# Performance work log

Hardware: AMD Instinct MI355X
Metric: run time of the kernel (lower is better)

The kernel has to match this reference:

```python
import jax, jax.numpy as jnp
import numpy as np

DIM = 1024
HEADS = 16
SCALE = DIM ** -0.5  # note: source scales by full dim, not head dim


def setup_inputs() -> dict:
    key = jax.random.key(0)
    k1, k2, k3 = jax.random.split(key, 3)
    b, n = 2, 2048
    x = jax.random.normal(k1, (b, n, DIM), dtype=jnp.float32)
    w_qkv = jax.random.normal(k2, (3 * DIM, DIM), dtype=jnp.float32) * (DIM ** -0.5)
    w_out = jax.random.normal(k3, (DIM, DIM), dtype=jnp.float32) * (DIM ** -0.5)
    b_out = jnp.zeros((DIM,), dtype=jnp.float32)
    return {"x": x, "w_qkv": w_qkv, "w_out": w_out, "b_out": b_out}


def reference(x, w_qkv, w_out, b_out):
    b, n, d = x.shape
    h = HEADS
    hd = d // h
    # torch Linear: y = x @ W.T
    qkv = x @ w_qkv.T  # [b, n, 3d]
    q, k, v = jnp.split(qkv, 3, axis=-1)
    # reshape to [b, h, n, hd]
    def to_heads(t):
        return t.reshape(b, n, h, hd).transpose(0, 2, 1, 3)
    q, k, v = to_heads(q), to_heads(k), to_heads(v)
    dots = jnp.einsum('bhqd,bhkd->bhqk', q, k) * SCALE
    attn = jax.nn.softmax(dots, axis=-1)
    out = jnp.einsum('bhqk,bhkd->bhqd', attn, v)
    out = out.transpose(0, 2, 1, 3).reshape(b, n, d)
    return out @ w_out.T + b_out
```

## Files before the change

kernel.cpp:

```cpp
#include <hip/hip_runtime.h>

typedef __attribute__((ext_vector_type(8))) _Float16 half8;
typedef __attribute__((ext_vector_type(4))) _Float16 half4;
typedef __attribute__((ext_vector_type(2))) __fp16 fp16x2;
typedef __attribute__((ext_vector_type(4))) float f32x4;
typedef __attribute__((ext_vector_type(4))) unsigned int u32x4;
typedef __attribute__((ext_vector_type(2))) unsigned int u32x2;

#define NSEQ 2048
#define DIMM 1024
#define NH   16
#define HD   64

typedef const void __attribute__((address_space(1))) gvoid_t;
typedef void __attribute__((address_space(3))) svoid_t;

__device__ __forceinline__ void gload_lds16(const void* g, void* l) {
  __builtin_amdgcn_global_load_lds((gvoid_t*)g, (svoid_t*)l, 16, 0, 0);
}

union H2U { fp16x2 h; unsigned int u; };

__global__ __launch_bounds__(256) void cvt_all(const float* __restrict__ x,
                                               const float* __restrict__ wqkv,
                                               const float* __restrict__ wout,
                                               _Float16* __restrict__ xh,
                                               _Float16* __restrict__ wqkvh,
                                               _Float16* __restrict__ wouth) {
  int i = blockIdx.x * 256 + threadIdx.x;
  const float* src;
  _Float16* dst;
  int off;
  if (i < 524288) { src = x; dst = xh; off = i; }
  else if (i < 917504) { src = wqkv; dst = wqkvh; off = i - 524288; }
  else { src = wout; dst = wouth; off = i - 917504; }
  const float4* p = (const float4*)src + (size_t)off * 2;
  float4 v0 = p[0], v1 = p[1];
  half8 h;
  h[0] = (_Float16)v0.x; h[1] = (_Float16)v0.y; h[2] = (_Float16)v0.z; h[3] = (_Float16)v0.w;
  h[4] = (_Float16)v1.x; h[5] = (_Float16)v1.y; h[6] = (_Float16)v1.z; h[7] = (_Float16)v1.w;
  *((half8*)dst + off) = h;
}

__device__ __forceinline__ void gemm_mainloop(const _Float16* __restrict__ A,
                                              const _Float16* __restrict__ B,
                                              int am0, int bn0,
                                              _Float16* As, _Float16* Bs,
                                              f32x4 acc[4][4]) {
  const int tid = threadIdx.x;
  const int w = tid >> 6, lane = tid & 63;
  const int lr = lane >> 2;
  const int lc = (lane & 3) * 8;
  const int wm = (w >> 1) * 64, wn = (w & 1) * 64;
  const int g = lane >> 4, ln = lane & 15;

  for (int k0 = 0; k0 < 1024; k0 += 32) {
#pragma unroll
    for (int rr = 0; rr < 4; ++rr) {
      int c = rr * 4 + w;
      if (c < 8) {
        gload_lds16(A + (size_t)(am0 + c * 16 + lr) * 1024 + k0 + lc, As + c * 512);
      } else {
        int cb = c - 8;
        gload_lds16(B + (size_t)(bn0 + cb * 16 + lr) * 1024 + k0 + lc, Bs + cb * 512);
      }
    }
    __syncthreads();
    half8 af[4], bf[4];
#pragma unroll
    for (int mi = 0; mi < 4; ++mi)
      af[mi] = *(const half8*)(As + (wm + mi * 16 + ln) * 32 + g * 8);
#pragma unroll
    for (int ni = 0; ni < 4; ++ni)
      bf[ni] = *(const half8*)(Bs + (wn + ni * 16 + ln) * 32 + g * 8);
#pragma unroll
    for (int mi = 0; mi < 4; ++mi)
#pragma unroll
      for (int ni = 0; ni < 4; ++ni)
        acc[mi][ni] = __builtin_amdgcn_mfma_f32_16x16x32_f16(af[mi], bf[ni], acc[mi][ni], 0, 0, 0);
    __syncthreads();
  }
}

union SmemQKV {
  struct { _Float16 a[128 * 32]; _Float16 b[128 * 32]; } ab;
  _Float16 t[128 * 136];
};

#define QSCALE 0.0450843450f

__global__ __launch_bounds__(256) void gemm_qkv(const _Float16* __restrict__ x,
                                                const _Float16* __restrict__ wqkv,
                                                _Float16* __restrict__ qh,
                                                _Float16* __restrict__ kh,
                                                _Float16* __restrict__ vt) {
  __shared__ SmemQKV sh;
  f32x4 acc[4][4];
#pragma unroll
  for (int i = 0; i < 4; ++i)
#pragma unroll
    for (int j = 0; j < 4; ++j) acc[i][j] = (f32x4){0.f, 0.f, 0.f, 0.f};
  const int bm = blockIdx.x, bn = blockIdx.y;
  gemm_mainloop(x, wqkv, bm * 128, bn * 128, sh.ab.a, sh.ab.b, acc);

  const int tid = threadIdx.x;
  const int w = tid >> 6, lane = tid & 63;
  const int g = lane >> 4, ln = lane & 15;
  const int wm = (w >> 1) * 64, wn = (w & 1) * 64;
  const int sec = bn >> 3;
  const int cbase = (bn & 7) * 128;

  if (sec < 2) {
    _Float16* dst = (sec == 0) ? qh : kh;
    const float scale = (sec == 0) ? QSCALE : 1.0f;
#pragma unroll
    for (int mi = 0; mi < 4; ++mi) {
      int row = bm * 128 + wm + mi * 16 + g * 4;
      int bidx = row >> 11, nidx = row & 2047;
#pragma unroll
      for (int ni = 0; ni < 4; ++ni) {
        int col = cbase + wn + ni * 16 + ln;
        int h = col >> 6, d = col & 63;
        _Float16* p = dst + ((size_t)(bidx * NH + h) * NSEQ + nidx) * HD + d;
#pragma unroll
        for (int r = 0; r < 4; ++r) p[r * HD] = (_Float16)(acc[mi][ni][r] * scale);
      }
    }
  } else {
    __syncthreads();
#pragma unroll
    for (int mi = 0; mi < 4; ++mi)
#pragma unroll
      for (int ni = 0; ni < 4; ++ni)
#pragma unroll
        for (int r = 0; r < 4; ++r)
          sh.t[(wn + ni * 16 + ln) * 136 + wm + mi * 16 + g * 4 + r] = (_Float16)acc[mi][ni][r];
    __syncthreads();
    const int row0 = bm * 128;
    const int bidx = row0 >> 11, n0 = row0 & 2047;
#pragma unroll
    for (int i = 0; i < 8; ++i) {
      int ci = i * 256 + tid;
      int drow = ci >> 4, nofs = (ci & 15) * 8;
      int col = cbase + drow;
      int h = col >> 6, d = col & 63;
      u32x4 val = *(const u32x4*)(sh.t + drow * 136 + nofs);
      *(u32x4*)(vt + ((size_t)(bidx * NH + h) * HD + d) * NSEQ + n0 + nofs) = val;
    }
  }
}

__global__ __launch_bounds__(256, 2) void attn_fwd(const _Float16* __restrict__ qh,
                                                   const _Float16* __restrict__ kh,
                                                   const _Float16* __restrict__ vt,
                                                   _Float16* __restrict__ ao) {
  __shared__ _Float16 Ks[2][64 * 64];
  __shared__ _Float16 Vs[2][64 * 64];
  __shared__ _Float16 Ps[4][32 * 64];

  const int bid = blockIdx.x;
  const int swz = (bid & 7) * 64 + (bid >> 3);
  const int bh = swz >> 4, qt = swz & 15;
  const int tid = threadIdx.x, w = tid >> 6, lane = tid & 63;
  const int g = lane >> 4, ln = lane & 15;
  const int sw8 = ln & 7;

  const _Float16* qp = qh + (size_t)bh * NSEQ * HD;
  const _Float16* kp = kh + (size_t)bh * NSEQ * HD;
  const _Float16* vp = vt + (size_t)bh * HD * NSEQ;
  char* psw = (char*)&Ps[w][0];

  const int qr = qt * 128 + w * 32;

  half8 qf[2][2];
#pragma unroll
  for (int qb = 0; qb < 2; ++qb)
#pragma unroll
    for (int dk = 0; dk < 2; ++dk)
      qf[qb][dk] = *(const half8*)(qp + (size_t)(qr + qb * 16 + ln) * HD + dk * 32 + g * 8);
  asm volatile("" ::: "memory");

  const int rsub = lane >> 3;
  const int csw = ((lane & 7) ^ rsub) << 3;
  const int c0 = 2 * w;

#define STAGE(buf, tt)                                                              \
  {                                                                                 \
    const _Float16* kt_ = kp + (size_t)(tt) * 64 * HD;                              \
    _Pragma("unroll")                                                               \
    for (int i = 0; i < 2; ++i) {                                                   \
      int c = c0 + i;                                                               \
      gload_lds16(kt_ + (size_t)(c * 8 + rsub) * HD + csw, &Ks[buf][c * 512]);      \
    }                                                                               \
    _Pragma("unroll")                                                               \
    for (int i = 0; i < 2; ++i) {                                                   \
      int c = c0 + i;                                                               \
      gload_lds16(vp + (size_t)(c * 8 + rsub) * NSEQ + (tt) * 64 + csw,             \
                  &Vs[buf][c * 512]);                                               \
    }                                                                               \
  }

  STAGE(0, 0);

  float lsum[2] = {0.f, 0.f};
  f32x4 oacc[4][2];
#pragma unroll
  for (int sd = 0; sd < 4; ++sd)
#pragma unroll
    for (int qb = 0; qb < 2; ++qb) oacc[sd][qb] = (f32x4){0.f, 0.f, 0.f, 0.f};
  const f32x4 fz = (f32x4){0.f, 0.f, 0.f, 0.f};

  for (int t = 0; t < 32; ++t) {
    const int cur = t & 1;
    STAGE(cur ^ 1, (t + 1) & 31);
    asm volatile("s_waitcnt vmcnt(4)" ::: "memory");
    __builtin_amdgcn_s_barrier();

    f32x4 sacc[4][2];
    __builtin_amdgcn_s_setprio(1);
#pragma unroll
    for (int s = 0; s < 4; ++s) {
      const _Float16* kb = &Ks[cur][(s * 16 + ln) * 64];
      half8 kf0 = *(const half8*)(kb + ((g ^ sw8) << 3));
      half8 kf1 = *(const half8*)(kb + (((4 + g) ^ sw8) << 3));
      sacc[s][0] = __builtin_amdgcn_mfma_f32_16x16x32_f16(kf0, qf[0][0], fz, 0, 0, 0);
      sacc[s][0] = __builtin_amdgcn_mfma_f32_16x16x32_f16(kf1, qf[0][1], sacc[s][0], 0, 0, 0);
      sacc[s][1] = __builtin_amdgcn_mfma_f32_16x16x32_f16(kf0, qf[1][0], fz, 0, 0, 0);
      sacc[s][1] = __builtin_amdgcn_mfma_f32_16x16x32_f16(kf1, qf[1][1], sacc[s][1], 0, 0, 0);
    }
    __builtin_amdgcn_s_setprio(0);

#pragma unroll
    for (int qb = 0; qb < 2; ++qb) {
      const int q = qb * 16 + ln;
      float rs = 0.f;
#pragma unroll
      for (int s = 0; s < 4; ++s) {
        float e0 = __builtin_amdgcn_exp2f(sacc[s][qb][0]);
        float e1 = __builtin_amdgcn_exp2f(sacc[s][qb][1]);
        float e2 = __builtin_amdgcn_exp2f(sacc[s][qb][2]);
        float e3 = __builtin_amdgcn_exp2f(sacc[s][qb][3]);
        rs += (e0 + e1) + (e2 + e3);
        H2U a, b2;
        a.h = __builtin_amdgcn_cvt_pkrtz(e0, e1);
        b2.h = __builtin_amdgcn_cvt_pkrtz(e2, e3);
        u32x2 quad; quad[0] = a.u; quad[1] = b2.u;
        const int kq = s * 4 + g;
        *(u32x2*)(psw + q * 128 + ((kq ^ ln) << 3)) = quad;
      }
      lsum[qb] += rs;
    }
    asm volatile("s_waitcnt lgkmcnt(0)" ::: "memory");

    half8 pb[2][2];
#pragma unroll
    for (int qb = 0; qb < 2; ++qb) {
      const int q = qb * 16 + ln;
#pragma unroll
      for (int f = 0; f < 2; ++f) {
        const int qd = (f * 4 + g) * 2;
        u32x2 lo = *(const u32x2*)(psw + q * 128 + ((qd ^ ln) << 3));
        u32x2 hi = *(const u32x2*)(psw + q * 128 + (((qd + 1) ^ ln) << 3));
        union { u32x4 u; half8 h; } pk;
        pk.u[0] = lo[0]; pk.u[1] = lo[1]; pk.u[2] = hi[0]; pk.u[3] = hi[1];
        pb[qb][f] = pk.h;
      }
    }

    __builtin_amdgcn_s_setprio(1);
#pragma unroll
    for (int sd = 0; sd < 4; ++sd) {
      const _Float16* vb = &Vs[cur][(sd * 16 + ln) * 64];
      half8 vf0 = *(const half8*)(vb + ((g ^ sw8) << 3));
      half8 vf1 = *(const half8*)(vb + (((4 + g) ^ sw8) << 3));
#pragma unroll
      for (int qb = 0; qb < 2; ++qb) {
        oacc[sd][qb] = __builtin_amdgcn_mfma_f32_16x16x32_f16(vf0, pb[qb][0], oacc[sd][qb], 0, 0, 0);
        oacc[sd][qb] = __builtin_amdgcn_mfma_f32_16x16x32_f16(vf1, pb[qb][1], oacc[sd][qb], 0, 0, 0);
      }
    }
    __builtin_amdgcn_s_setprio(0);

    asm volatile("s_waitcnt lgkmcnt(0)" ::: "memory");
    __builtin_amdgcn_s_barrier();
  }

  const int bidx = bh >> 4, h = bh & 15;
#pragma unroll
  for (int qb = 0; qb < 2; ++qb) {
    lsum[qb] += __shfl_xor(lsum[qb], 16, 64);
    lsum[qb] += __shfl_xor(lsum[qb], 32, 64);
    const float inv = 1.f / lsum[qb];
    const int n = qr + qb * 16 + ln;
#pragma unroll
    for (int sd = 0; sd < 4; ++sd) {
      half4 o4;
#pragma unroll
      for (int r = 0; r < 4; ++r) o4[r] = (_Float16)(oacc[sd][qb][r] * inv);
      *(half4*)(ao + (size_t)(bidx * NSEQ + n) * DIMM + h * HD + sd * 16 + g * 4) = o4;
    }
  }
}

__global__ __launch_bounds__(256) void gemm_out(const _Float16* __restrict__ ao,
                                                const _Float16* __restrict__ wout,
                                                const float* __restrict__ bias,
                                                float* __restrict__ out) {
  __shared__ _Float16 As[128 * 32];
  __shared__ _Float16 Bs[128 * 32];
  f32x4 acc[4][4];
#pragma unroll
  for (int i = 0; i < 4; ++i)
#pragma unroll
    for (int j = 0; j < 4; ++j) acc[i][j] = (f32x4){0.f, 0.f, 0.f, 0.f};
  const int bm = blockIdx.x, bn = blockIdx.y;
  gemm_mainloop(ao, wout, bm * 128, bn * 128, As, Bs, acc);
  const int tid = threadIdx.x;
  const int w = tid >> 6, lane = tid & 63;
  const int g = lane >> 4, ln = lane & 15;
  const int wm = (w >> 1) * 64, wn = (w & 1) * 64;
#pragma unroll
  for (int mi = 0; mi < 4; ++mi) {
    const int row = bm * 128 + wm + mi * 16 + g * 4;
#pragma unroll
    for (int ni = 0; ni < 4; ++ni) {
      const int col = bn * 128 + wn + ni * 16 + ln;
      const float b = bias[col];
#pragma unroll
      for (int r = 0; r < 4; ++r) out[(size_t)(row + r) * DIMM + col] = acc[mi][ni][r] + b;
    }
  }
}

extern "C" void kernel_launch(void* const* d_in, const int* in_sizes, int n_in,
                              void* d_out, int out_size, void* d_ws, size_t ws_size,
                              hipStream_t stream) {
  const float* x    = (const float*)d_in[0];
  const float* wqkv = (const float*)d_in[1];
  const float* wout = (const float*)d_in[2];
  const float* bout = (const float*)d_in[3];
  float* out = (float*)d_out;

  _Float16* ws = (_Float16*)d_ws;
  _Float16* x_h    = ws;
  _Float16* wqkv_h = ws + (4u << 20);
  _Float16* wout_h = ws + (7u << 20);
  _Float16* q_h    = ws + (8u << 20);
  _Float16* k_h    = ws + (12u << 20);
  _Float16* vt_h   = ws + (16u << 20);
  _Float16* ao_h   = ws + (20u << 20);

  cvt_all<<<dim3(4096), 256, 0, stream>>>(x, wqkv, wout, x_h, wqkv_h, wout_h);
  gemm_qkv<<<dim3(32, 24), 256, 0, stream>>>(x_h, wqkv_h, q_h, k_h, vt_h);
  attn_fwd<<<dim3(512), 256, 0, stream>>>(q_h, k_h, vt_h, ao_h);
  gemm_out<<<dim3(32, 8), 256, 0, stream>>>(ao_h, wout_h, bout, out);
}
```

Baseline: 115.9 us.

## Split attention waves across key halves with 64-row query blocks and LDS reduction

Restructures the attention work split so each wave handles 64 query rows against one 32-key half of each K/V tile, instead of 32 query rows against the full tile. Each wave now loads fewer K/V fragments from LDS per MFMA and reads its P fragment as a single 16-byte load, which cuts LDS traffic and removes the packing shuffles. At the end, the two key-half partial outputs and row sums are combined through a shared-memory union buffer. The cost is more accumulator registers per wave (16 f32x4 output tiles), an extra end-of-kernel LDS reduction with a sync, and a risk of lower occupancy under launch_bounds(256,2).

```diff
diff --git a/kernel.cpp b/kernel.cpp
--- a/kernel.cpp
+++ b/kernel.cpp
@@ -150,13 +150,19 @@
   }
 }
 
-__global__ __launch_bounds__(256, 2) void attn_fwd(const _Float16* __restrict__ qh,
-                                                   const _Float16* __restrict__ kh,
-                                                   const _Float16* __restrict__ vt,
+union SmemPO {
+  _Float16 P[4][64 * 40];
+  float O[2][64][64];
+};
+
+__global__ __launch_bounds__(256, 2) void attn_fwd(const _Float16* __restrict__ qg,
+                                                   const _Float16* __restrict__ kg,
+                                                   const _Float16* __restrict__ vg,
                                                    _Float16* __restrict__ ao) {
   __shared__ _Float16 Ks[2][64 * 64];
   __shared__ _Float16 Vs[2][64 * 64];
-  __shared__ _Float16 Ps[4][32 * 64];
+  __shared__ SmemPO PO;
+  __shared__ float Lred[2][128];
 
   const int bid = blockIdx.x;
   const int swz = (bid & 7) * 64 + (bid >> 3);
@@ -164,20 +170,23 @@
   const int tid = threadIdx.x, w = tid >> 6, lane = tid & 63;
   const int g = lane >> 4, ln = lane & 15;
   const int sw8 = ln & 7;
-
-  const _Float16* qp = qh + (size_t)bh * NSEQ * HD;
-  const _Float16* kp = kh + (size_t)bh * NSEQ * HD;
-  const _Float16* vp = vt + (size_t)bh * HD * NSEQ;
-  char* psw = (char*)&Ps[w][0];
-
-  const int qr = qt * 128 + w * 32;
-
-  half8 qf[2][2];
-#pragma unroll
-  for (int qb = 0; qb < 2; ++qb)
+  const int kh2 = w & 1;
+  const int qh2 = w >> 1;
+  const int koff = kh2 * 32;
+
+  const _Float16* qp = qg + (size_t)bh * NSEQ * HD;
+  const _Float16* kp = kg + (size_t)bh * NSEQ * HD;
+  const _Float16* vp = vg + (size_t)bh * HD * NSEQ;
+  char* psw = (char*)&PO.P[w][0];
+
+  const int qr0 = qt * 128;
+
+  half8 qf[4][2];
+#pragma unroll
+  for (int qb = 0; qb < 4; ++qb)
 #pragma unroll
     for (int dk = 0; dk < 2; ++dk)
-      qf[qb][dk] = *(const half8*)(qp + (size_t)(qr + qb * 16 + ln) * HD + dk * 32 + g * 8);
+      qf[qb][dk] = *(const half8*)(qp + (size_t)(qr0 + qh2 * 64 + qb * 16 + ln) * HD + dk * 32 + g * 8);
   asm volatile("" ::: "memory");
 
   const int rsub = lane >> 3;
@@ -202,12 +211,12 @@
 
   STAGE(0, 0);
 
-  float lsum[2] = {0.f, 0.f};
-  f32x4 oacc[4][2];
-#pragma unroll
-  for (int sd = 0; sd < 4; ++sd)
-#pragma unroll
-    for (int qb = 0; qb < 2; ++qb) oacc[sd][qb] = (f32x4){0.f, 0.f, 0.f, 0.f};
+  float lsum[4] = {0.f, 0.f, 0.f, 0.f};
+  f32x4 oacc[4][4];
+#pragma unroll
+  for (int db = 0; db < 4; ++db)
+#pragma unroll
+    for (int qb = 0; qb < 4; ++qb) oacc[db][qb] = (f32x4){0.f, 0.f, 0.f, 0.f};
   const f32x4 fz = (f32x4){0.f, 0.f, 0.f, 0.f};
 
   for (int t = 0; t < 32; ++t) {
@@ -216,68 +225,58 @@
     asm volatile("s_waitcnt vmcnt(4)" ::: "memory");
     __builtin_amdgcn_s_barrier();
 
-    f32x4 sacc[4][2];
+    half8 kf[2][2];
+#pragma unroll
+    for (int kb = 0; kb < 2; ++kb)
+#pragma unroll
+      for (int dk = 0; dk < 2; ++dk)
+        kf[kb][dk] = *(const half8*)(&Ks[cur][0] + (koff + kb * 16 + ln) * 64 +
+                                     (((dk * 4 + g) ^ sw8) << 3));
+    f32x4 sacc[2][4];
     __builtin_amdgcn_s_setprio(1);
 #pragma unroll
-    for (int s = 0; s < 4; ++s) {
-      const _Float16* kb = &Ks[cur][(s * 16 + ln) * 64];
-      half8 kf0 = *(const half8*)(kb + ((g ^ sw8) << 3));
-      half8 kf1 = *(const half8*)(kb + (((4 + g) ^ sw8) << 3));
-      sacc[s][0] = __builtin_amdgcn_mfma_f32_16x16x32_f16(kf0, qf[0][0], fz, 0, 0, 0);
-      sacc[s][0] = __builtin_amdgcn_mfma_f32_16x16x32_f16(kf1, qf[0][1], sacc[s][0], 0, 0, 0);
-      sacc[s][1] = __builtin_amdgcn_mfma_f32_16x16x32_f16(kf0, qf[1][0], fz, 0, 0, 0);
-      sacc[s][1] = __builtin_amdgcn_mfma_f32_16x16x32_f16(kf1, qf[1][1], sacc[s][1], 0, 0, 0);
-    }
+    for (int kb = 0; kb < 2; ++kb)
+#pragma unroll
+      for (int qb = 0; qb < 4; ++qb) {
+        sacc[kb][qb] = __builtin_amdgcn_mfma_f32_16x16x32_f16(kf[kb][0], qf[qb][0], fz, 0, 0, 0);
+        sacc[kb][qb] = __builtin_amdgcn_mfma_f32_16x16x32_f16(kf[kb][1], qf[qb][1], sacc[kb][qb], 0, 0, 0);
+      }
     __builtin_amdgcn_s_setprio(0);
 
 #pragma unroll
-    for (int qb = 0; qb < 2; ++qb) {
+    for (int qb = 0; qb < 4; ++qb) {
       const int q = qb * 16 + ln;
       float rs = 0.f;
 #pragma unroll
-      for (int s = 0; s < 4; ++s) {
-        float e0 = __builtin_amdgcn_exp2f(sacc[s][qb][0]);
-        float e1 = __builtin_amdgcn_exp2f(sacc[s][qb][1]);
-        float e2 = __builtin_amdgcn_exp2f(sacc[s][qb][2]);
-        float e3 = __builtin_amdgcn_exp2f(sacc[s][qb][3]);
+      for (int kb = 0; kb < 2; ++kb) {
+        float e0 = __builtin_amdgcn_exp2f(sacc[kb][qb][0]);
+        float e1 = __builtin_amdgcn_exp2f(sacc[kb][qb][1]);
+        float e2 = __builtin_amdgcn_exp2f(sacc[kb][qb][2]);
+        float e3 = __builtin_amdgcn_exp2f(sacc[kb][qb][3]);
         rs += (e0 + e1) + (e2 + e3);
         H2U a, b2;
         a.h = __builtin_amdgcn_cvt_pkrtz(e0, e1);
         b2.h = __builtin_amdgcn_cvt_pkrtz(e2, e3);
         u32x2 quad; quad[0] = a.u; quad[1] = b2.u;
-        const int kq = s * 4 + g;
-        *(u32x2*)(psw + q * 128 + ((kq ^ ln) << 3)) = quad;
+        *(u32x2*)(psw + q * 80 + kb * 32 + g * 8) = quad;
       }
       lsum[qb] += rs;
     }
     asm volatile("s_waitcnt lgkmcnt(0)" ::: "memory");
 
-    half8 pb[2][2];
-#pragma unroll
-    for (int qb = 0; qb < 2; ++qb) {
-      const int q = qb * 16 + ln;
-#pragma unroll
-      for (int f = 0; f < 2; ++f) {
-        const int qd = (f * 4 + g) * 2;
-        u32x2 lo = *(const u32x2*)(psw + q * 128 + ((qd ^ ln) << 3));
-        u32x2 hi = *(const u32x2*)(psw + q * 128 + (((qd + 1) ^ ln) << 3));
-        union { u32x4 u; half8 h; } pk;
-        pk.u[0] = lo[0]; pk.u[1] = lo[1]; pk.u[2] = hi[0]; pk.u[3] = hi[1];
-        pb[qb][f] = pk.h;
-      }
-    }
+    half8 pbf[4];
+#pragma unroll
+    for (int qb = 0; qb < 4; ++qb)
+      pbf[qb] = *(const half8*)(psw + (qb * 16 + ln) * 80 + g * 16);
 
     __builtin_amdgcn_s_setprio(1);
 #pragma unroll
-    for (int sd = 0; sd < 4; ++sd) {
-      const _Float16* vb = &Vs[cur][(sd * 16 + ln) * 64];
-      half8 vf0 = *(const half8*)(vb + ((g ^ sw8) << 3));
-      half8 vf1 = *(const half8*)(vb + (((4 + g) ^ sw8) << 3));
-#pragma unroll
-      for (int qb = 0; qb < 2; ++qb) {
-        oacc[sd][qb] = __builtin_amdgcn_mfma_f32_16x16x32_f16(vf0, pb[qb][0], oacc[sd][qb], 0, 0, 0);
-        oacc[sd][qb] = __builtin_amdgcn_mfma_f32_16x16x32_f16(vf1, pb[qb][1], oacc[sd][qb], 0, 0, 0);
-      }
+    for (int db = 0; db < 4; ++db) {
+      half8 vf = *(const half8*)(&Vs[cur][0] + (db * 16 + ln) * 64 +
+                                 (((kh2 * 4 + g) ^ sw8) << 3));
+#pragma unroll
+      for (int qb = 0; qb < 4; ++qb)
+        oacc[db][qb] = __builtin_amdgcn_mfma_f32_16x16x32_f16(vf, pbf[qb], oacc[db][qb], 0, 0, 0);
     }
     __builtin_amdgcn_s_setprio(0);
 
@@ -285,19 +284,47 @@
     __builtin_amdgcn_s_barrier();
   }
 
-  const int bidx = bh >> 4, h = bh & 15;
-#pragma unroll
-  for (int qb = 0; qb < 2; ++qb) {
+#pragma unroll
+  for (int qb = 0; qb < 4; ++qb) {
     lsum[qb] += __shfl_xor(lsum[qb], 16, 64);
     lsum[qb] += __shfl_xor(lsum[qb], 32, 64);
-    const float inv = 1.f / lsum[qb];
-    const int n = qr + qb * 16 + ln;
-#pragma unroll
-    for (int sd = 0; sd < 4; ++sd) {
-      half4 o4;
-#pragma unroll
-      for (int r = 0; r < 4; ++r) o4[r] = (_Float16)(oacc[sd][qb][r] * inv);
-      *(half4*)(ao + (size_t)(bidx * NSEQ + n) * DIMM + h * HD + sd * 16 + g * 4) = o4;
+  }
+  if (g == 0) {
+#pragma unroll
+    for (int qb = 0; qb < 4; ++qb)
+      Lred[kh2][qh2 * 64 + qb * 16 + ln] = lsum[qb];
+  }
+  if (kh2) {
+#pragma unroll
+    for (int db = 0; db < 4; ++db)
+#pragma unroll
+      for (int qb = 0; qb < 4; ++qb)
+#pragma unroll
+        for (int r = 0; r < 4; ++r)
+          PO.O[qh2][db * 16 + g * 4 + r][qb * 16 + ln] = oacc[db][qb][r];
+  }
+  __syncthreads();
+  if (!kh2) {
+    const int bidx = bh >> 4, h = bh & 15;
+    float inv[4];
+#pragma unroll
+    for (int qb = 0; qb < 4; ++qb) {
+      const int q = qh2 * 64 + qb * 16 + ln;
+      inv[qb] = 1.f / (Lred[0][q] + Lred[1][q]);
+    }
+#pragma unroll
+    for (int qb = 0; qb < 4; ++qb) {
+      const int n = qr0 + qh2 * 64 + qb * 16 + ln;
+#pragma unroll
+      for (int db = 0; db < 4; ++db) {
+        half4 o4;
+#pragma unroll
+        for (int r = 0; r < 4; ++r) {
+          float v = oacc[db][qb][r] + PO.O[qh2][db * 16 + g * 4 + r][qb * 16 + ln];
+          o4[r] = (_Float16)(v * inv[qb]);
+        }
+        *(half4*)(ao + (size_t)(bidx * NSEQ + n) * DIMM + h * HD + db * 16 + g * 4) = o4;
+      }
     }
   }
 }
```

After: 114.8 us. No clear change (-0.9%).

## Split attention key tiles across wave pairs and double grid with LDS reduction

Applied to the files above, without the earlier changes.

Each attention block now handles 64 queries instead of 128. Its four waves form two query halves times two key halves, and each wave processes 32 of the 64 keys per tile. Partial outputs and row sums from the second key half are reduced through LDS, in a union reusing the K buffer, before the final normalize and store. The grid doubles to 1024 blocks, the occupancy hint rises to 4 blocks per CU, and the last tile is peeled to avoid a redundant prefetch. This buys more parallelism and smaller per-wave register and LDS footprints, at the cost of twice the K/V staging traffic per query and an extra reduction step.

```diff
diff --git a/kernel.cpp b/kernel.cpp
--- a/kernel.cpp
+++ b/kernel.cpp
@@ -150,34 +150,42 @@
   }
 }
 
-__global__ __launch_bounds__(256, 2) void attn_fwd(const _Float16* __restrict__ qh,
-                                                   const _Float16* __restrict__ kh,
-                                                   const _Float16* __restrict__ vt,
+union KOU {
+  _Float16 K[2][64 * 64];
+  float O[2][32][64];
+};
+
+__global__ __launch_bounds__(256, 4) void attn_fwd(const _Float16* __restrict__ qg,
+                                                   const _Float16* __restrict__ kg,
+                                                   const _Float16* __restrict__ vg,
                                                    _Float16* __restrict__ ao) {
-  __shared__ _Float16 Ks[2][64 * 64];
+  __shared__ KOU ku;
   __shared__ _Float16 Vs[2][64 * 64];
-  __shared__ _Float16 Ps[4][32 * 64];
+  __shared__ _Float16 Ps[4][1024];
 
   const int bid = blockIdx.x;
-  const int swz = (bid & 7) * 64 + (bid >> 3);
-  const int bh = swz >> 4, qt = swz & 15;
+  const int swz = (bid & 7) * 128 + (bid >> 3);
+  const int bh = swz >> 5, qt = swz & 31;
   const int tid = threadIdx.x, w = tid >> 6, lane = tid & 63;
   const int g = lane >> 4, ln = lane & 15;
   const int sw8 = ln & 7;
-
-  const _Float16* qp = qh + (size_t)bh * NSEQ * HD;
-  const _Float16* kp = kh + (size_t)bh * NSEQ * HD;
-  const _Float16* vp = vt + (size_t)bh * HD * NSEQ;
+  const int kh2 = w & 1, qh2 = w >> 1;
+  const int koff = kh2 * 32;
+  const int pkey = (ln >> 1) & 6;
+
+  const _Float16* qp = qg + (size_t)bh * NSEQ * HD;
+  const _Float16* kp = kg + (size_t)bh * NSEQ * HD;
+  const _Float16* vp = vg + (size_t)bh * HD * NSEQ;
   char* psw = (char*)&Ps[w][0];
 
-  const int qr = qt * 128 + w * 32;
+  const int qr0 = qt * 64;
 
   half8 qf[2][2];
 #pragma unroll
   for (int qb = 0; qb < 2; ++qb)
 #pragma unroll
     for (int dk = 0; dk < 2; ++dk)
-      qf[qb][dk] = *(const half8*)(qp + (size_t)(qr + qb * 16 + ln) * HD + dk * 32 + g * 8);
+      qf[qb][dk] = *(const half8*)(qp + (size_t)(qr0 + qh2 * 32 + qb * 16 + ln) * HD + dk * 32 + g * 8);
   asm volatile("" ::: "memory");
 
   const int rsub = lane >> 3;
@@ -190,7 +198,7 @@
     _Pragma("unroll")                                                               \
     for (int i = 0; i < 2; ++i) {                                                   \
       int c = c0 + i;                                                               \
-      gload_lds16(kt_ + (size_t)(c * 8 + rsub) * HD + csw, &Ks[buf][c * 512]);      \
+      gload_lds16(kt_ + (size_t)(c * 8 + rsub) * HD + csw, &ku.K[buf][c * 512]);    \
     }                                                                               \
     _Pragma("unroll")                                                               \
     for (int i = 0; i < 2; ++i) {                                                   \
@@ -205,99 +213,117 @@
   float lsum[2] = {0.f, 0.f};
   f32x4 oacc[4][2];
 #pragma unroll
-  for (int sd = 0; sd < 4; ++sd)
-#pragma unroll
-    for (int qb = 0; qb < 2; ++qb) oacc[sd][qb] = (f32x4){0.f, 0.f, 0.f, 0.f};
+  for (int db = 0; db < 4; ++db)
+#pragma unroll
+    for (int qb = 0; qb < 2; ++qb) oacc[db][qb] = (f32x4){0.f, 0.f, 0.f, 0.f};
   const f32x4 fz = (f32x4){0.f, 0.f, 0.f, 0.f};
 
-  for (int t = 0; t < 32; ++t) {
+#define TILE_BODY(cur)                                                              \
+  {                                                                                 \
+    half8 kf[2][2];                                                                 \
+    _Pragma("unroll")                                                               \
+    for (int kb = 0; kb < 2; ++kb)                                                  \
+      _Pragma("unroll")                                                             \
+      for (int dk = 0; dk < 2; ++dk)                                                \
+        kf[kb][dk] = *(const half8*)(&ku.K[cur][0] + (koff + kb * 16 + ln) * 64 +   \
+                                     (((dk * 4 + g) ^ sw8) << 3));                  \
+    f32x4 sacc[2][2];                                                               \
+    __builtin_amdgcn_s_setprio(1);                                                  \
+    _Pragma("unroll")                                                               \
+    for (int kb = 0; kb < 2; ++kb)                                                  \
+      _Pragma("unroll")                                                             \
+      for (int qb = 0; qb < 2; ++qb) {                                              \
+        sacc[kb][qb] = __builtin_amdgcn_mfma_f32_16x16x32_f16(kf[kb][0], qf[qb][0], fz, 0, 0, 0); \
+        sacc[kb][qb] = __builtin_amdgcn_mfma_f32_16x16x32_f16(kf[kb][1], qf[qb][1], sacc[kb][qb], 0, 0, 0); \
+      }                                                                             \
+    __builtin_amdgcn_s_setprio(0);                                                  \
+    _Pragma("unroll")                                                               \
+    for (int qb = 0; qb < 2; ++qb) {                                                \
+      const int q = qb * 16 + ln;                                                   \
+      float rs = 0.f;                                                               \
+      _Pragma("unroll")                                                             \
+      for (int kb = 0; kb < 2; ++kb) {                                              \
+        float e0 = __builtin_amdgcn_exp2f(sacc[kb][qb][0]);                         \
+        float e1 = __builtin_amdgcn_exp2f(sacc[kb][qb][1]);                         \
+        float e2 = __builtin_amdgcn_exp2f(sacc[kb][qb][2]);                         \
+        float e3 = __builtin_amdgcn_exp2f(sacc[kb][qb][3]);                         \
+        rs += (e0 + e1) + (e2 + e3);                                                \
+        H2U a_, b_;                                                                 \
+        a_.h = __builtin_amdgcn_cvt_pkrtz(e0, e1);                                  \
+        b_.h = __builtin_amdgcn_cvt_pkrtz(e2, e3);                                  \
+        u32x2 quad; quad[0] = a_.u; quad[1] = b_.u;                                 \
+        *(u32x2*)(psw + q * 64 + (((kb * 4 + g) ^ pkey) << 3)) = quad;              \
+      }                                                                             \
+      lsum[qb] += rs;                                                               \
+    }                                                                               \
+    asm volatile("s_waitcnt lgkmcnt(0)" ::: "memory");                              \
+    half8 pbf[2];                                                                   \
+    _Pragma("unroll")                                                               \
+    for (int qb = 0; qb < 2; ++qb)                                                  \
+      pbf[qb] = *(const half8*)(psw + (qb * 16 + ln) * 64 + (((2 * g) ^ pkey) << 3)); \
+    __builtin_amdgcn_s_setprio(1);                                                  \
+    _Pragma("unroll")                                                               \
+    for (int db = 0; db < 4; ++db) {                                                \
+      half8 vf = *(const half8*)(&Vs[cur][0] + (db * 16 + ln) * 64 +                \
+                                 (((kh2 * 4 + g) ^ sw8) << 3));                     \
+      _Pragma("unroll")                                                             \
+      for (int qb = 0; qb < 2; ++qb)                                                \
+        oacc[db][qb] = __builtin_amdgcn_mfma_f32_16x16x32_f16(vf, pbf[qb], oacc[db][qb], 0, 0, 0); \
+    }                                                                               \
+    __builtin_amdgcn_s_setprio(0);                                                  \
+  }
+
+  for (int t = 0; t < 31; ++t) {
     const int cur = t & 1;
-    STAGE(cur ^ 1, (t + 1) & 31);
+    STAGE(cur ^ 1, t + 1);
     asm volatile("s_waitcnt vmcnt(4)" ::: "memory");
     __builtin_amdgcn_s_barrier();
-
-    f32x4 sacc[4][2];
-    __builtin_amdgcn_s_setprio(1);
-#pragma unroll
-    for (int s = 0; s < 4; ++s) {
-      const _Float16* kb = &Ks[cur][(s * 16 + ln) * 64];
-      half8 kf0 = *(const half8*)(kb + ((g ^ sw8) << 3));
-      half8 kf1 = *(const half8*)(kb + (((4 + g) ^ sw8) << 3));
-      sacc[s][0] = __builtin_amdgcn_mfma_f32_16x16x32_f16(kf0, qf[0][0], fz, 0, 0, 0);
-      sacc[s][0] = __builtin_amdgcn_mfma_f32_16x16x32_f16(kf1, qf[0][1], sacc[s][0], 0, 0, 0);
-      sacc[s][1] = __builtin_amdgcn_mfma_f32_16x16x32_f16(kf0, qf[1][0], fz, 0, 0, 0);
-      sacc[s][1] = __builtin_amdgcn_mfma_f32_16x16x32_f16(kf1, qf[1][1], sacc[s][1], 0, 0, 0);
-    }
-    __builtin_amdgcn_s_setprio(0);
-
-#pragma unroll
-    for (int qb = 0; qb < 2; ++qb) {
-      const int q = qb * 16 + ln;
-      float rs = 0.f;
-#pragma unroll
-      for (int s = 0; s < 4; ++s) {
-        float e0 = __builtin_amdgcn_exp2f(sacc[s][qb][0]);
-        float e1 = __builtin_amdgcn_exp2f(sacc[s][qb][1]);
-        float e2 = __builtin_amdgcn_exp2f(sacc[s][qb][2]);
-        float e3 = __builtin_amdgcn_exp2f(sacc[s][qb][3]);
-        rs += (e0 + e1) + (e2 + e3);
-        H2U a, b2;
-        a.h = __builtin_amdgcn_cvt_pkrtz(e0, e1);
-        b2.h = __builtin_amdgcn_cvt_pkrtz(e2, e3);
-        u32x2 quad; quad[0] = a.u; quad[1] = b2.u;
-        const int kq = s * 4 + g;
-        *(u32x2*)(psw + q * 128 + ((kq ^ ln) << 3)) = quad;
-      }
-      lsum[qb] += rs;
-    }
-    asm volatile("s_waitcnt lgkmcnt(0)" ::: "memory");
-
-    half8 pb[2][2];
-#pragma unroll
-    for (int qb = 0; qb < 2; ++qb) {
-      const int q = qb * 16 + ln;
-#pragma unroll
-      for (int f = 0; f < 2; ++f) {
-        const int qd = (f * 4 + g) * 2;
-        u32x2 lo = *(const u32x2*)(psw + q * 128 + ((qd ^ ln) << 3));
-        u32x2 hi = *(const u32x2*)(psw + q * 128 + (((qd + 1) ^ ln) << 3));
-        union { u32x4 u; half8 h; } pk;
-        pk.u[0] = lo[0]; pk.u[1] = lo[1]; pk.u[2] = hi[0]; pk.u[3] = hi[1];
-        pb[qb][f] = pk.h;
-      }
-    }
-
-    __builtin_amdgcn_s_setprio(1);
-#pragma unroll
-    for (int sd = 0; sd < 4; ++sd) {
-      const _Float16* vb = &Vs[cur][(sd * 16 + ln) * 64];
-      half8 vf0 = *(const half8*)(vb + ((g ^ sw8) << 3));
-      half8 vf1 = *(const half8*)(vb + (((4 + g) ^ sw8) << 3));
-#pragma unroll
-      for (int qb = 0; qb < 2; ++qb) {
-        oacc[sd][qb] = __builtin_amdgcn_mfma_f32_16x16x32_f16(vf0, pb[qb][0], oacc[sd][qb], 0, 0, 0);
-        oacc[sd][qb] = __builtin_amdgcn_mfma_f32_16x16x32_f16(vf1, pb[qb][1], oacc[sd][qb], 0, 0, 0);
-      }
-    }
-    __builtin_amdgcn_s_setprio(0);
-
+    TILE_BODY(cur)
     asm volatile("s_waitcnt lgkmcnt(0)" ::: "memory");
     __builtin_amdgcn_s_barrier();
   }
-
-  const int bidx = bh >> 4, h = bh & 15;
+  {
+    asm volatile("s_waitcnt vmcnt(0)" ::: "memory");
+    __builtin_amdgcn_s_barrier();
+    TILE_BODY(1)
+    asm volatile("s_waitcnt lgkmcnt(0)" ::: "memory");
+    __builtin_amdgcn_s_barrier();
+  }
+
 #pragma unroll
   for (int qb = 0; qb < 2; ++qb) {
     lsum[qb] += __shfl_xor(lsum[qb], 16, 64);
     lsum[qb] += __shfl_xor(lsum[qb], 32, 64);
-    const float inv = 1.f / lsum[qb];
-    const int n = qr + qb * 16 + ln;
-#pragma unroll
-    for (int sd = 0; sd < 4; ++sd) {
-      half4 o4;
-#pragma unroll
-      for (int r = 0; r < 4; ++r) o4[r] = (_Float16)(oacc[sd][qb][r] * inv);
-      *(half4*)(ao + (size_t)(bidx * NSEQ + n) * DIMM + h * HD + sd * 16 + g * 4) = o4;
+  }
+  float* Lred = (float*)&Ps[0][0];
+  if (kh2) {
+    if (g == 0) {
+#pragma unroll
+      for (int qb = 0; qb < 2; ++qb)
+        Lred[qh2 * 32 + qb * 16 + ln] = lsum[qb];
+    }
+#pragma unroll
+    for (int db = 0; db < 4; ++db)
+#pragma unroll
+      for (int qb = 0; qb < 2; ++qb)
+        *(f32x4*)&ku.O[qh2][qb * 16 + ln][db * 16 + g * 4] = oacc[db][qb];
+  }
+  __syncthreads();
+  if (!kh2) {
+    const int bidx = bh >> 4, h = bh & 15;
+#pragma unroll
+    for (int qb = 0; qb < 2; ++qb) {
+      const int q = qh2 * 32 + qb * 16 + ln;
+      const float inv = 1.f / (lsum[qb] + Lred[q]);
+      const int n = qr0 + q;
+#pragma unroll
+      for (int db = 0; db < 4; ++db) {
+        f32x4 part = *(const f32x4*)&ku.O[qh2][qb * 16 + ln][db * 16 + g * 4];
+        half4 o4;
+#pragma unroll
+        for (int r = 0; r < 4; ++r) o4[r] = (_Float16)((oacc[db][qb][r] + part[r]) * inv);
+        *(half4*)(ao + (size_t)(bidx * NSEQ + n) * DIMM + h * HD + db * 16 + g * 4) = o4;
+      }
     }
   }
 }
@@ -352,6 +378,6 @@
 
   cvt_all<<<dim3(4096), 256, 0, stream>>>(x, wqkv, wout, x_h, wqkv_h, wout_h);
   gemm_qkv<<<dim3(32, 24), 256, 0, stream>>>(x_h, wqkv_h, q_h, k_h, vt_h);
-  attn_fwd<<<dim3(512), 256, 0, stream>>>(q_h, k_h, vt_h, ao_h);
+  attn_fwd<<<dim3(1024), 256, 0, stream>>>(q_h, k_h, vt_h, ao_h);
   gemm_out<<<dim3(32, 8), 256, 0, stream>>>(ao_h, wout_h, bout, out);
 }
```

After: 135.7 us. 1.17x slower.
